# Kernel optimization log

Measured on AMD Instinct MI355X. Metric: run time of the kernel, lower is better.

The kernel has to match this reference:

```python
import jax, jax.numpy as jnp
import numpy as np

NEG_INF = -1.0e9
LN_EPS = 1e-5
LEAK = 0.2


def setup_inputs() -> dict:
    key = jax.random.key(0)
    ks = jax.random.split(key, 8)
    B, C, T, N, H = 8, 64, 24, 512, 2
    hd = C // H
    x = jax.random.normal(ks[0], (B, C, T, N), dtype=jnp.float32)
    gso = jax.random.randint(ks[1], (N, N), 0, 2, dtype=jnp.int32)
    # torch nn.Linear weights are (out, in); xavier-ish scale
    s = (2.0 / (C + C)) ** 0.5
    Wq = jax.random.normal(ks[2], (C, C), dtype=jnp.float32) * s
    Wk = jax.random.normal(ks[3], (C, C), dtype=jnp.float32) * s
    Wv = jax.random.normal(ks[4], (C, C), dtype=jnp.float32) * s
    sa = (2.0 / (H + hd)) ** 0.5
    a_src = jax.random.normal(ks[5], (H, hd), dtype=jnp.float32) * sa
    a_dst = jax.random.normal(ks[6], (H, hd), dtype=jnp.float32) * sa
    ln_gamma = jnp.ones((C,), dtype=jnp.float32)
    ln_beta = jnp.zeros((C,), dtype=jnp.float32)
    return {"x": x, "gso": gso, "Wq": Wq, "Wk": Wk, "Wv": Wv,
            "a_src": a_src, "a_dst": a_dst, "ln_gamma": ln_gamma, "ln_beta": ln_beta}


def _spatial_gat(x, gso, Wq, Wk, Wv, a_src, a_dst, ln_gamma, ln_beta):
    B, C, T, N = x.shape
    H, hd = a_src.shape
    # (B, C, T, N) -> (B*T, N, C)
    xr = jnp.transpose(x, (0, 2, 3, 1)).reshape(B * T, N, C)
    # torch Linear: y = x @ W.T
    Q = jnp.einsum('bnc,dc->bnd', xr, Wq).reshape(B * T, N, H, hd)
    K = jnp.einsum('bnc,dc->bnd', xr, Wk).reshape(B * T, N, H, hd)
    V = jnp.einsum('bnc,dc->bnd', xr, Wv).reshape(B * T, N, H, hd)
    # additive GAT scores, all heads at once
    s_src = jnp.einsum('bnhd,hd->bnh', Q, a_src)  # (BT, N, H)
    s_dst = jnp.einsum('bnhd,hd->bnh', K, a_dst)  # (BT, N, H)
    scores = jax.nn.leaky_relu(s_src[:, :, None, :] + s_dst[:, None, :, :], LEAK)  # (BT, Ni, Nj, H)
    mask = jnp.where(gso == 0, jnp.float32(NEG_INF), jnp.float32(0.0))  # (N, N)
    scores = scores + mask[None, :, :, None]
    attn = jax.nn.softmax(scores, axis=2)  # softmax over destination j
    out = jnp.einsum('bijh,bjhd->bihd', attn, V)  # (BT, N, H, hd)
    out = out.reshape(B * T, N, C)
    # LayerNorm over channel dim
    mu = jnp.mean(out, axis=-1, keepdims=True)
    var = jnp.var(out, axis=-1, keepdims=True)
    out = (out - mu) * jax.lax.rsqrt(var + LN_EPS) * ln_gamma + ln_beta
    # back to (B, C, T, N)
    return jnp.transpose(out.reshape(B, T, N, C), (0, 3, 1, 2))


def reference(x, gso, Wq, Wk, Wv, a_src, a_dst, ln_gamma, ln_beta):
    return _spatial_gat(x, gso, Wq, Wk, Wv, a_src, a_dst, ln_gamma, ln_beta)
```

## Files before the change

kernel.cpp:

```cpp
#include <hip/hip_runtime.h>

#define CDIM 64
#define TDIM 24
#define NDIM 512
#define NBT  192

typedef float    float4v __attribute__((ext_vector_type(4)));
typedef _Float16 half8v  __attribute__((ext_vector_type(8)));
typedef _Float16 half4v  __attribute__((ext_vector_type(4)));
typedef _Float16 half2v  __attribute__((ext_vector_type(2)));


__device__ __forceinline__ float exp2_fast(float x) {
#if __has_builtin(__builtin_amdgcn_exp2f)
  return __builtin_amdgcn_exp2f(x);
#else
  return __expf(x * 0.69314718f);
#endif
}

struct SmemK1 {
  union {
    _Float16 xt[128][72];
    _Float16 vtb[64][136];
  } big;
  _Float16 wv[64][72];
  _Float16 wext[16][72];
};

__launch_bounds__(256, 4)
__global__ void k1_v(const float* __restrict__ x,  const float* __restrict__ Wv,
                     const float* __restrict__ Wq, const float* __restrict__ Wk,
                     const float* __restrict__ a_src, const float* __restrict__ a_dst,
                     const int* __restrict__ gso,
                     _Float16* __restrict__ VT_g,
                     _Float16* __restrict__ F16, _Float16* __restrict__ P16,
                     _Float16* __restrict__ E16, _Float16* __restrict__ Q16,
                     unsigned char* __restrict__ maskb) {
  const int t  = threadIdx.x;
  const int bx = blockIdx.x;

  if (bx >= 768) {
    int g = (bx - 768) * 256 + t;
    const int4* gp = (const int4*)gso + (size_t)g * 4;
    unsigned w[4];
#pragma unroll
    for (int k = 0; k < 4; ++k) {
      int4 v = gp[k];
      w[k] = (v.x ? 0x000000FFu : 0u) | (v.y ? 0x0000FF00u : 0u) |
             (v.z ? 0x00FF0000u : 0u) | (v.w ? 0xFF000000u : 0u);
    }
    uint4 o; o.x = w[0]; o.y = w[1]; o.z = w[2]; o.w = w[3];
    ((uint4*)maskb)[g] = o;
    return;
  }

  __shared__ SmemK1 sm;
  const int qn = bx & 3;
  const int bt = bx >> 2;
  const int b  = bt / TDIM, tt = bt % TDIM;
  const int n0 = qn * 128;

#pragma unroll
  for (int it = 0; it < 4; ++it) {
    int idx = it * 256 + t;
    float4 vv = ((const float4*)Wv)[idx];
    int d = idx >> 4, k4 = (idx & 15) * 4;
    half4v h4; h4[0] = (_Float16)vv.x; h4[1] = (_Float16)vv.y;
    h4[2] = (_Float16)vv.z; h4[3] = (_Float16)vv.w;
    *(half4v*)&sm.wv[d][k4] = h4;
  }
  for (int z = t; z < 12 * 72; z += 256) ((_Float16*)sm.wext[4])[z] = (_Float16)0.f;
  if (t < 64) {
    int c = t;
    float s0 = 0.f, s1 = 0.f, d0 = 0.f, d1 = 0.f;
#pragma unroll
    for (int d = 0; d < 32; ++d) {
      s0 += a_src[d]      * Wq[d * 64 + c];
      s1 += a_src[32 + d] * Wq[(32 + d) * 64 + c];
      d0 += a_dst[d]      * Wk[d * 64 + c];
      d1 += a_dst[32 + d] * Wk[(32 + d) * 64 + c];
    }
    const float l2e = 1.44269504f;
    sm.wext[0][c] = (_Float16)(s0 * l2e); sm.wext[1][c] = (_Float16)(s1 * l2e);
    sm.wext[2][c] = (_Float16)(d0 * l2e); sm.wext[3][c] = (_Float16)(d1 * l2e);
  }
  for (int it = 0; it < 16; ++it) {
    int idx = it * 256 + t;
    int cp = idx >> 7, n = idx & 127;
    int c0 = cp * 2;
    const float* base = x + ((size_t)(b * CDIM + c0) * TDIM + tt) * NDIM + n0 + n;
    half2v p; p[0] = (_Float16)base[0]; p[1] = (_Float16)base[(size_t)TDIM * NDIM];
    *(half2v*)&sm.big.xt[n][c0] = p;
  }
  __syncthreads();

  const int lane = t & 63, w = t >> 6;
  const int m = lane & 15, quad = lane >> 4;
  const int mbase = w * 32;

  float4v acc[2][5];
#pragma unroll
  for (int mt = 0; mt < 2; ++mt)
#pragma unroll
    for (int nt = 0; nt < 5; ++nt)
#pragma unroll
      for (int r = 0; r < 4; ++r) acc[mt][nt][r] = 0.f;

#pragma unroll
  for (int ks = 0; ks < 2; ++ks) {
    half8v af[2], bf[5];
#pragma unroll
    for (int mt = 0; mt < 2; ++mt)
      af[mt] = *(const half8v*)&sm.big.xt[mbase + mt * 16 + m][ks * 32 + quad * 8];
#pragma unroll
    for (int nt = 0; nt < 4; ++nt)
      bf[nt] = *(const half8v*)&sm.wv[nt * 16 + m][ks * 32 + quad * 8];
    bf[4] = *(const half8v*)&sm.wext[m][ks * 32 + quad * 8];
#pragma unroll
    for (int mt = 0; mt < 2; ++mt)
#pragma unroll
      for (int nt = 0; nt < 5; ++nt)
        acc[mt][nt] = __builtin_amdgcn_mfma_f32_16x16x32_f16(af[mt], bf[nt], acc[mt][nt], 0, 0, 0);
  }

  if (m < 4) {
    const int hh = m & 1;
    const bool is_src = (m < 2);
    _Float16* eb = (is_src ? E16 : F16) + ((size_t)(bt * 2 + hh)) * NDIM;
    _Float16* qb = (is_src ? Q16 : P16) + ((size_t)(bt * 2 + hh)) * NDIM;
    const float bias = is_src ? -6.f : 0.f;
#pragma unroll
    for (int mt = 0; mt < 2; ++mt)
#pragma unroll
      for (int r = 0; r < 4; ++r) {
        float s = acc[mt][4][r];
        int n = n0 + mbase + mt * 16 + quad * 4 + r;
        eb[n] = (_Float16)exp2_fast(s + bias);
        qb[n] = (_Float16)exp2_fast(0.2f * s + bias);
      }
  }
  __syncthreads();

#pragma unroll
  for (int mt = 0; mt < 2; ++mt)
#pragma unroll
    for (int nt = 0; nt < 4; ++nt)
#pragma unroll
      for (int r = 0; r < 4; r += 2) {
        int nl = mbase + mt * 16 + quad * 4 + r;
        int c  = nt * 16 + m;
        half2v p = __builtin_bit_cast(half2v,
            __builtin_amdgcn_cvt_pkrtz(acc[mt][nt][r], acc[mt][nt][r + 1]));
        *(half2v*)&sm.big.vtb[c][nl] = p;
      }
  __syncthreads();

  const uint4* vq = (const uint4*)sm.big.vtb;
#pragma unroll
  for (int it = 0; it < 4; ++it) {
    int idx = it * 256 + t;
    int c = idx >> 4, q4 = idx & 15;
    ((uint4*)VT_g)[(size_t)(bt * 64 + c) * 64 + qn * 16 + q4] = vq[c * 17 + q4];
  }
}

struct SmemK2 {
  union {
    struct { _Float16 vt[2][64][128]; } s;
    struct { float otile[128][66]; float rsum[2][128]; float rsq[2][128];
             float mu[128]; float rs[128]; } e;
  } u;
  _Float16 sF16[2][512];
  _Float16 sP16[2][512];
};

__launch_bounds__(256, 3)
__global__ void k2_attn(const _Float16* __restrict__ VT_g,
                        const _Float16* __restrict__ F16, const _Float16* __restrict__ P16,
                        const _Float16* __restrict__ E16, const _Float16* __restrict__ Q16,
                        const unsigned char* __restrict__ maskb,
                        const float* __restrict__ gamma, const float* __restrict__ beta,
                        float* __restrict__ out) {
  __shared__ SmemK2 sm;
  const int t     = threadIdx.x;
  const int id    = blockIdx.x;
  const int itile = (id >> 3) & 3;
  const int bt    = ((id >> 5) << 3) | (id & 7);
  const int i0    = itile * 128;
  const int b     = bt / TDIM, tt = bt % TDIM;
  const int lane  = t & 63, w = t >> 6;
  const int h = w >> 1, ihalf = w & 1;
  const int m = lane & 15, quad = lane >> 4;
  const int rbase = ihalf * 64;

  {
    uint2 fv = ((const uint2*)(F16 + (size_t)bt * 2 * NDIM))[t];
    uint2 pw = ((const uint2*)(P16 + (size_t)bt * 2 * NDIM))[t];
    ((uint2*)sm.sF16)[t] = fv;
    ((uint2*)sm.sP16)[t] = pw;
  }
  half2v e2[4], q2[4];
  {
    const _Float16* eb = E16 + ((size_t)(bt * 2 + h)) * NDIM + i0 + rbase + m;
    const _Float16* qb = Q16 + ((size_t)(bt * 2 + h)) * NDIM + i0 + rbase + m;
#pragma unroll
    for (int mt = 0; mt < 4; ++mt) {
      _Float16 ev = eb[mt * 16];
      _Float16 qv = qb[mt * 16];
      e2[mt][0] = ev; e2[mt][1] = ev;
      q2[mt][0] = qv; q2[mt][1] = qv;
    }
  }

  float4v acc[4][2], accs[4];
#pragma unroll
  for (int mt = 0; mt < 4; ++mt)
#pragma unroll
    for (int r = 0; r < 4; ++r) { acc[mt][0][r] = 0.f; acc[mt][1][r] = 0.f; accs[mt][r] = 0.f; }
  const half8v bones = {(_Float16)1.f, (_Float16)1.f, (_Float16)1.f, (_Float16)1.f,
                        (_Float16)1.f, (_Float16)1.f, (_Float16)1.f, (_Float16)1.f};

  const uint4* vsrc = (const uint4*)VT_g;
  uint4 pv0, pv1, pv2, pv3;
  const int vc  = t >> 4;
  const int vch = t & 15;
  const int vswz = (vch * 8) ^ ((vc & 7) * 8);

  const unsigned char* mrow = maskb + (size_t)(i0 + rbase + m) * NDIM + quad * 8;
  uint2 mk[4][4];

#define PREFETCH_V(js_)                                                        \
  { pv0 = vsrc[(size_t)(bt * 64 + vc     ) * 64 + (js_) * 16 + vch];           \
    pv1 = vsrc[(size_t)(bt * 64 + vc + 16) * 64 + (js_) * 16 + vch];           \
    pv2 = vsrc[(size_t)(bt * 64 + vc + 32) * 64 + (js_) * 16 + vch];           \
    pv3 = vsrc[(size_t)(bt * 64 + vc + 48) * 64 + (js_) * 16 + vch]; }

#define PREFETCH_M(js_)                                                        \
  { _Pragma("unroll")                                                          \
    for (int mt = 0; mt < 4; ++mt) {                                           \
      const unsigned char* mbp = mrow + (size_t)(mt * 16) * NDIM + (js_) * 128;\
      _Pragma("unroll")                                                        \
      for (int ksl = 0; ksl < 4; ++ksl)                                        \
        mk[mt][ksl] = *(const uint2*)(mbp + ksl * 32);                         \
    } }

#define COMMIT(buf_)                                                           \
  { *(uint4*)&sm.u.s.vt[buf_][vc     ][vswz] = pv0;                            \
    *(uint4*)&sm.u.s.vt[buf_][vc + 16][vswz] = pv1;                            \
    *(uint4*)&sm.u.s.vt[buf_][vc + 32][vswz] = pv2;                            \
    *(uint4*)&sm.u.s.vt[buf_][vc + 48][vswz] = pv3; }

#define SLICE(buf_, js_, ksl_)                                                 \
  {                                                                            \
    const int jq = (ksl_) * 32 + quad * 8;                                     \
    half8v F8 = *(const half8v*)&sm.sF16[h][(js_) * 128 + jq];                 \
    half8v P8 = *(const half8v*)&sm.sP16[h][(js_) * 128 + jq];                 \
    const int vbase = (h * 32 + m) * 128 + (jq ^ ((m & 7) * 8));               \
    half8v b0 = *(const half8v*)&sm.u.s.vt[buf_][0][vbase];                    \
    half8v b1 = *(const half8v*)&sm.u.s.vt[buf_][0][vbase + 16 * 128];         \
    uint4 fu = __builtin_bit_cast(uint4, F8);                                  \
    uint4 pu = __builtin_bit_cast(uint4, P8);                                  \
    half2v f2a = __builtin_bit_cast(half2v, fu.x), f2b = __builtin_bit_cast(half2v, fu.y); \
    half2v f2c = __builtin_bit_cast(half2v, fu.z), f2d = __builtin_bit_cast(half2v, fu.w); \
    half2v p2a = __builtin_bit_cast(half2v, pu.x), p2b = __builtin_bit_cast(half2v, pu.y); \
    half2v p2c = __builtin_bit_cast(half2v, pu.z), p2d = __builtin_bit_cast(half2v, pu.w); \
    _Pragma("unroll")                                                          \
    for (int mt = 0; mt < 4; ++mt) {                                           \
      unsigned mw0 = mk[mt][ksl_].x, mw1 = mk[mt][ksl_].y;                     \
      uint4 eu;                                                                \
      eu.x = __builtin_bit_cast(unsigned,                                      \
               __builtin_elementwise_max(e2[mt] * f2a, q2[mt] * p2a)) &        \
             __builtin_amdgcn_perm(0u, mw0, 0x01010000u);                      \
      eu.y = __builtin_bit_cast(unsigned,                                      \
               __builtin_elementwise_max(e2[mt] * f2b, q2[mt] * p2b)) &        \
             __builtin_amdgcn_perm(0u, mw0, 0x03030202u);                      \
      eu.z = __builtin_bit_cast(unsigned,                                      \
               __builtin_elementwise_max(e2[mt] * f2c, q2[mt] * p2c)) &        \
             __builtin_amdgcn_perm(0u, mw1, 0x01010000u);                      \
      eu.w = __builtin_bit_cast(unsigned,                                      \
               __builtin_elementwise_max(e2[mt] * f2d, q2[mt] * p2d)) &        \
             __builtin_amdgcn_perm(0u, mw1, 0x03030202u);                      \
      half8v af = __builtin_bit_cast(half8v, eu);                              \
      acc[mt][0] = __builtin_amdgcn_mfma_f32_16x16x32_f16(af, b0,    acc[mt][0], 0, 0, 0); \
      acc[mt][1] = __builtin_amdgcn_mfma_f32_16x16x32_f16(af, b1,    acc[mt][1], 0, 0, 0); \
      accs[mt]   = __builtin_amdgcn_mfma_f32_16x16x32_f16(af, bones, accs[mt],   0, 0, 0); \
    }                                                                          \
  }

  PREFETCH_V(0);
  PREFETCH_M(0);
  COMMIT(0);
  __syncthreads();

#pragma unroll
  for (int js = 0; js < 4; ++js) {
    const int cur = js & 1, nxt = cur ^ 1;
    if (js < 3) PREFETCH_V(js + 1);
    SLICE(cur, js, 0);
    SLICE(cur, js, 1);
    SLICE(cur, js, 2);
    SLICE(cur, js, 3);
    if (js < 3) {
      PREFETCH_M(js + 1);
      COMMIT(nxt);
      __syncthreads();
    }
  }
#undef SLICE
#undef COMMIT
#undef PREFETCH_M
#undef PREFETCH_V

  __syncthreads();
#pragma unroll
  for (int mt = 0; mt < 4; ++mt)
#pragma unroll
    for (int r = 0; r < 4; ++r) {
      float sc = __builtin_amdgcn_rcpf(accs[mt][r]);
      int i_loc = rbase + mt * 16 + quad * 4 + r;
#pragma unroll
      for (int nt = 0; nt < 2; ++nt)
        sm.u.e.otile[i_loc][h * 32 + nt * 16 + m] = acc[mt][nt][r] * sc;
    }
  __syncthreads();

  {
    int i = t & 127, cg = t >> 7;
    float s1 = 0.f, s2 = 0.f;
#pragma unroll
    for (int cc = 0; cc < 32; ++cc) {
      float v = sm.u.e.otile[i][cg * 32 + cc];
      s1 += v; s2 += v * v;
    }
    sm.u.e.rsum[cg][i] = s1;
    sm.u.e.rsq[cg][i]  = s2;
  }
  __syncthreads();
  if (t < 128) {
    int i = t;
    float s1 = sm.u.e.rsum[0][i] + sm.u.e.rsum[1][i];
    float s2 = sm.u.e.rsq[0][i]  + sm.u.e.rsq[1][i];
    float mu  = s1 * (1.f / 64.f);
    float var = s2 * (1.f / 64.f) - mu * mu;
    sm.u.e.mu[i] = mu;
    sm.u.e.rs[i] = rsqrtf(var + 1e-5f);
  }
  __syncthreads();
  {
    int i = t & 127, cg = t >> 7;
    float mu = sm.u.e.mu[i], rs = sm.u.e.rs[i];
    int n = i0 + i;
#pragma unroll
    for (int cc = 0; cc < 32; ++cc) {
      int c = cg * 32 + cc;
      float v = (sm.u.e.otile[i][c] - mu) * rs * gamma[c] + beta[c];
      out[((size_t)(b * CDIM + c) * TDIM + tt) * NDIM + n] = v;
    }
  }
}

extern "C" void kernel_launch(void* const* d_in, const int* in_sizes, int n_in,
                              void* d_out, int out_size, void* d_ws, size_t ws_size,
                              hipStream_t stream) {
  const float* x     = (const float*)d_in[0];
  const int*   gso   = (const int*)d_in[1];
  const float* Wq    = (const float*)d_in[2];
  const float* Wk    = (const float*)d_in[3];
  const float* Wv    = (const float*)d_in[4];
  const float* a_src = (const float*)d_in[5];
  const float* a_dst = (const float*)d_in[6];
  const float* gamma = (const float*)d_in[7];
  const float* beta  = (const float*)d_in[8];
  float* out = (float*)d_out;

  char* ws = (char*)d_ws;
  _Float16* VT_g = (_Float16*)ws;
  _Float16* F16  = (_Float16*)(ws + 12582912);
  _Float16* P16  = (_Float16*)(ws + 12976128);
  _Float16* E16  = (_Float16*)(ws + 13369344);
  _Float16* Q16  = (_Float16*)(ws + 13762560);
  unsigned char* maskb = (unsigned char*)(ws + 14155776);

  k1_v<<<832, 256, 0, stream>>>(x, Wv, Wq, Wk, a_src, a_dst, gso,
                                VT_g, F16, P16, E16, Q16, maskb);
  k2_attn<<<768, 256, 0, stream>>>(VT_g, F16, P16, E16, Q16, maskb,
                                   gamma, beta, out);
}
```

Baseline: 124.4 us.

## Move exp2 of GAT scores into attention kernel and single-buffer V tile

k1 now writes raw fp32 source/destination scores instead of four precomputed fp16 exponential arrays. k2 computes the exp2 terms itself when loading them. k2 also drops the double-buffered V tile in shared memory for a single buffer with two barriers per quarter. Mask prefetch is now ping-ponged between two register sets and issued mid-quarter. This cuts shared memory, which may allow more blocks per CU, and moves the exp work out of k1. In exchange it adds exp work in every k2 block, plus extra barriers that serialize the V commit with compute.

```diff
diff --git a/kernel.cpp b/kernel.cpp
--- a/kernel.cpp
+++ b/kernel.cpp
@@ -34,8 +34,7 @@
                      const float* __restrict__ a_src, const float* __restrict__ a_dst,
                      const int* __restrict__ gso,
                      _Float16* __restrict__ VT_g,
-                     _Float16* __restrict__ F16, _Float16* __restrict__ P16,
-                     _Float16* __restrict__ E16, _Float16* __restrict__ Q16,
+                     float* __restrict__ s_src_g, float* __restrict__ s_dst_g,
                      unsigned char* __restrict__ maskb) {
   const int t  = threadIdx.x;
   const int bx = blockIdx.x;
@@ -125,20 +124,12 @@
   }
 
   if (m < 4) {
-    const int hh = m & 1;
-    const bool is_src = (m < 2);
-    _Float16* eb = (is_src ? E16 : F16) + ((size_t)(bt * 2 + hh)) * NDIM;
-    _Float16* qb = (is_src ? Q16 : P16) + ((size_t)(bt * 2 + hh)) * NDIM;
-    const float bias = is_src ? -6.f : 0.f;
+    float* basep = (m < 2 ? s_src_g : s_dst_g) + (size_t)(bt * 2 + (m & 1)) * NDIM;
 #pragma unroll
     for (int mt = 0; mt < 2; ++mt)
 #pragma unroll
-      for (int r = 0; r < 4; ++r) {
-        float s = acc[mt][4][r];
-        int n = n0 + mbase + mt * 16 + quad * 4 + r;
-        eb[n] = (_Float16)exp2_fast(s + bias);
-        qb[n] = (_Float16)exp2_fast(0.2f * s + bias);
-      }
+      for (int r = 0; r < 4; ++r)
+        basep[n0 + mbase + mt * 16 + quad * 4 + r] = acc[mt][4][r];
   }
   __syncthreads();
 
@@ -167,7 +158,7 @@
 
 struct SmemK2 {
   union {
-    struct { _Float16 vt[2][64][128]; } s;
+    struct { _Float16 vt[64][128]; } s;
     struct { float otile[128][66]; float rsum[2][128]; float rsq[2][128];
              float mu[128]; float rs[128]; } e;
   } u;
@@ -177,8 +168,7 @@
 
 __launch_bounds__(256, 3)
 __global__ void k2_attn(const _Float16* __restrict__ VT_g,
-                        const _Float16* __restrict__ F16, const _Float16* __restrict__ P16,
-                        const _Float16* __restrict__ E16, const _Float16* __restrict__ Q16,
+                        const float* __restrict__ s_src_g, const float* __restrict__ s_dst_g,
                         const unsigned char* __restrict__ maskb,
                         const float* __restrict__ gamma, const float* __restrict__ beta,
                         float* __restrict__ out) {
@@ -194,23 +184,20 @@
   const int m = lane & 15, quad = lane >> 4;
   const int rbase = ihalf * 64;
 
-  {
-    uint2 fv = ((const uint2*)(F16 + (size_t)bt * 2 * NDIM))[t];
-    uint2 pw = ((const uint2*)(P16 + (size_t)bt * 2 * NDIM))[t];
-    ((uint2*)sm.sF16)[t] = fv;
-    ((uint2*)sm.sP16)[t] = pw;
+  for (int it = 0; it < 4; ++it) {
+    int idx = it * 256 + t;
+    float d = s_dst_g[(size_t)bt * 2 * NDIM + idx];
+    ((_Float16*)sm.sF16)[idx] = (_Float16)exp2_fast(d);
+    ((_Float16*)sm.sP16)[idx] = (_Float16)exp2_fast(0.2f * d);
   }
   half2v e2[4], q2[4];
-  {
-    const _Float16* eb = E16 + ((size_t)(bt * 2 + h)) * NDIM + i0 + rbase + m;
-    const _Float16* qb = Q16 + ((size_t)(bt * 2 + h)) * NDIM + i0 + rbase + m;
-#pragma unroll
-    for (int mt = 0; mt < 4; ++mt) {
-      _Float16 ev = eb[mt * 16];
-      _Float16 qv = qb[mt * 16];
-      e2[mt][0] = ev; e2[mt][1] = ev;
-      q2[mt][0] = qv; q2[mt][1] = qv;
-    }
+#pragma unroll
+  for (int mt = 0; mt < 4; ++mt) {
+    float sv = s_src_g[(size_t)(bt * 2 + h) * NDIM + i0 + rbase + mt * 16 + m];
+    _Float16 ev = (_Float16)exp2_fast(sv - 6.f);
+    _Float16 qv = (_Float16)exp2_fast(0.2f * sv - 6.f);
+    e2[mt][0] = ev; e2[mt][1] = ev;
+    q2[mt][0] = qv; q2[mt][1] = qv;
   }
 
   float4v acc[4][2], accs[4];
@@ -228,7 +215,7 @@
   const int vswz = (vch * 8) ^ ((vc & 7) * 8);
 
   const unsigned char* mrow = maskb + (size_t)(i0 + rbase + m) * NDIM + quad * 8;
-  uint2 mk[4][4];
+  uint2 mkA[4][4], mkB[4][4];
 
 #define PREFETCH_V(js_)                                                        \
   { pv0 = vsrc[(size_t)(bt * 64 + vc     ) * 64 + (js_) * 16 + vch];           \
@@ -236,29 +223,23 @@
     pv2 = vsrc[(size_t)(bt * 64 + vc + 32) * 64 + (js_) * 16 + vch];           \
     pv3 = vsrc[(size_t)(bt * 64 + vc + 48) * 64 + (js_) * 16 + vch]; }
 
-#define PREFETCH_M(js_)                                                        \
+#define PREFETCH_M(mk_, js_)                                                   \
   { _Pragma("unroll")                                                          \
     for (int mt = 0; mt < 4; ++mt) {                                           \
       const unsigned char* mbp = mrow + (size_t)(mt * 16) * NDIM + (js_) * 128;\
       _Pragma("unroll")                                                        \
       for (int ksl = 0; ksl < 4; ++ksl)                                        \
-        mk[mt][ksl] = *(const uint2*)(mbp + ksl * 32);                         \
+        mk_[mt][ksl] = *(const uint2*)(mbp + ksl * 32);                        \
     } }
 
-#define COMMIT(buf_)                                                           \
-  { *(uint4*)&sm.u.s.vt[buf_][vc     ][vswz] = pv0;                            \
-    *(uint4*)&sm.u.s.vt[buf_][vc + 16][vswz] = pv1;                            \
-    *(uint4*)&sm.u.s.vt[buf_][vc + 32][vswz] = pv2;                            \
-    *(uint4*)&sm.u.s.vt[buf_][vc + 48][vswz] = pv3; }
-
-#define SLICE(buf_, js_, ksl_)                                                 \
+#define SLICE(mk_, js_, ksl_)                                                  \
   {                                                                            \
     const int jq = (ksl_) * 32 + quad * 8;                                     \
     half8v F8 = *(const half8v*)&sm.sF16[h][(js_) * 128 + jq];                 \
     half8v P8 = *(const half8v*)&sm.sP16[h][(js_) * 128 + jq];                 \
     const int vbase = (h * 32 + m) * 128 + (jq ^ ((m & 7) * 8));               \
-    half8v b0 = *(const half8v*)&sm.u.s.vt[buf_][0][vbase];                    \
-    half8v b1 = *(const half8v*)&sm.u.s.vt[buf_][0][vbase + 16 * 128];         \
+    half8v b0 = *(const half8v*)&sm.u.s.vt[0][vbase];                          \
+    half8v b1 = *(const half8v*)&sm.u.s.vt[0][vbase + 16 * 128];               \
     uint4 fu = __builtin_bit_cast(uint4, F8);                                  \
     uint4 pu = __builtin_bit_cast(uint4, P8);                                  \
     half2v f2a = __builtin_bit_cast(half2v, fu.x), f2b = __builtin_bit_cast(half2v, fu.y); \
@@ -267,7 +248,7 @@
     half2v p2c = __builtin_bit_cast(half2v, pu.z), p2d = __builtin_bit_cast(half2v, pu.w); \
     _Pragma("unroll")                                                          \
     for (int mt = 0; mt < 4; ++mt) {                                           \
-      unsigned mw0 = mk[mt][ksl_].x, mw1 = mk[mt][ksl_].y;                     \
+      unsigned mw0 = mk_[mt][ksl_].x, mw1 = mk_[mt][ksl_].y;                   \
       uint4 eu;                                                                \
       eu.x = __builtin_bit_cast(unsigned,                                      \
                __builtin_elementwise_max(e2[mt] * f2a, q2[mt] * p2a)) &        \
@@ -289,26 +270,30 @@
   }
 
   PREFETCH_V(0);
-  PREFETCH_M(0);
-  COMMIT(0);
-  __syncthreads();
-
-#pragma unroll
-  for (int js = 0; js < 4; ++js) {
-    const int cur = js & 1, nxt = cur ^ 1;
-    if (js < 3) PREFETCH_V(js + 1);
-    SLICE(cur, js, 0);
-    SLICE(cur, js, 1);
-    SLICE(cur, js, 2);
-    SLICE(cur, js, 3);
-    if (js < 3) {
-      PREFETCH_M(js + 1);
-      COMMIT(nxt);
-      __syncthreads();
-    }
-  }
+  PREFETCH_M(mkA, 0);
+
+#define QUARTER(mkX_, mkY_, js_)                                               \
+  {                                                                            \
+    __syncthreads();                          \
+    *(uint4*)&sm.u.s.vt[vc     ][vswz] = pv0;                                  \
+    *(uint4*)&sm.u.s.vt[vc + 16][vswz] = pv1;                                  \
+    *(uint4*)&sm.u.s.vt[vc + 32][vswz] = pv2;                                  \
+    *(uint4*)&sm.u.s.vt[vc + 48][vswz] = pv3;                                  \
+    __syncthreads();                                                           \
+    if ((js_) < 3) PREFETCH_V((js_) + 1);                                      \
+    SLICE(mkX_, js_, 0);                                                       \
+    SLICE(mkX_, js_, 1);                                                       \
+    if ((js_) < 3) PREFETCH_M(mkY_, (js_) + 1);                                \
+    SLICE(mkX_, js_, 2);                                                       \
+    SLICE(mkX_, js_, 3);                                                       \
+  }
+
+  QUARTER(mkA, mkB, 0);
+  QUARTER(mkB, mkA, 1);
+  QUARTER(mkA, mkB, 2);
+  QUARTER(mkB, mkA, 3);
+#undef QUARTER
 #undef SLICE
-#undef COMMIT
 #undef PREFETCH_M
 #undef PREFETCH_V
 
@@ -375,15 +360,12 @@
   float* out = (float*)d_out;
 
   char* ws = (char*)d_ws;
-  _Float16* VT_g = (_Float16*)ws;
-  _Float16* F16  = (_Float16*)(ws + 12582912);
-  _Float16* P16  = (_Float16*)(ws + 12976128);
-  _Float16* E16  = (_Float16*)(ws + 13369344);
-  _Float16* Q16  = (_Float16*)(ws + 13762560);
+  _Float16* VT_g  = (_Float16*)ws;
+  float*    s_src = (float*)(ws + 12582912);
+  float*    s_dst = (float*)(ws + 13369344);
   unsigned char* maskb = (unsigned char*)(ws + 14155776);
 
   k1_v<<<832, 256, 0, stream>>>(x, Wv, Wq, Wk, a_src, a_dst, gso,
-                                VT_g, F16, P16, E16, Q16, maskb);
-  k2_attn<<<768, 256, 0, stream>>>(VT_g, F16, P16, E16, Q16, maskb,
-                                   gamma, beta, out);
+                                VT_g, s_src, s_dst, maskb);
+  k2_attn<<<768, 256, 0, stream>>>(VT_g, s_src, s_dst, maskb, gamma, beta, out);
 }
```

Result: no change. 126.6 us (+1.8%).
